# Kernel optimization log

Measured on AMD Instinct MI355X. Metric: run time of the kernel, lower is better.

The kernel has to match this reference:

```python
import jax, jax.numpy as jnp
import numpy as np

LM_TEMP = 2.0      # opts.lm_temp
LAMBDA_SH = 20.0   # lambda_sh passed in ot_loss
EPS = 1e-8


def sinkhorn(M, a, b, lam, num_iter_max=1000, stop_thr=0.005):
    """Faithful port of sinkhorn_pytorch. M:[S,V], a:[S,B], b:[V,B]."""
    K = jnp.exp(-M * lam)          # [S,V]
    KM = K * M
    u0 = jnp.ones_like(a) / a.shape[0]
    v0 = jnp.zeros_like(b)

    def cond(state):
        cpt, u, v, err = state
        return (cpt < num_iter_max) & (err > stop_thr)

    def body(state):
        cpt, u, v, err = state
        u = a / (K @ (b / (u.T @ K).T))   # fused fixed-point step
        cpt = cpt + 1
        do_check = ((cpt % 20) == 1) | (cpt == num_iter_max)

        def check(uve):
            u, v, _ = uve
            v = b / (K.T @ u)
            u = a / (K @ v)
            bb = v * (K.T @ u)
            err = jnp.max(jnp.sum(jnp.abs(bb - b), axis=0))  # inf-norm over batch
            return u, v, err

        u, v, err = jax.lax.cond(do_check, check, lambda t: t, (u, v, err))
        return cpt, u, v, err

    state0 = (jnp.asarray(0, jnp.int32), u0, v0, jnp.asarray(1.0, M.dtype))
    _, u, v, _ = jax.lax.while_loop(cond, body, state0)
    return jnp.sum(u * (KM @ v), axis=0)   # [B] sinkhorn divergences


def setup_inputs() -> dict:
    key = jax.random.key(0)
    ks = jax.random.split(key, 6)
    B, H, V, NV, MAX_SLOTS = 512, 1024, 28996, 3000, 33
    inputs = jax.random.normal(ks[0], (B, 2 * H), jnp.float32)
    outputs = jax.random.normal(ks[1], (B, 512), jnp.float32)
    W_lm = jax.random.normal(ks[2], (V, H), jnp.float32) * 0.02   # lm head (no bias)
    W_lin = jax.random.normal(ks[3], (MAX_SLOTS, 512), jnp.float32) * 0.05
    b_lin = jnp.zeros((MAX_SLOTS,), jnp.float32)
    topics = jax.random.normal(ks[4], (MAX_SLOTS - 1, H), jnp.float32) * 0.01
    verbs = jax.random.randint(ks[5], (NV,), 0, V)
    return {"inputs": inputs, "outputs": outputs, "W_lm": W_lm,
            "W_lin": W_lin, "b_lin": b_lin, "topics": topics,
            "verbs": verbs, "nslots": 33}


def reference(inputs, outputs, W_lm, W_lin, b_lin, topics, verbs, nslots):
    H = W_lm.shape[1]
    # gather verb rows of the lm head once: logits[:, verbs] == x @ W_lm[verbs].T
    W_v = W_lm[verbs]                               # [NV, H]
    Wt = W_v.T                                      # [H, NV]
    o11 = jax.nn.softmax((inputs[:, :H] @ Wt) / LM_TEMP, axis=-1)
    o12 = jax.nn.softmax((inputs[:, H:] @ Wt) / LM_TEMP, axis=-1)
    o1 = (o11 + o12) * 0.5
    o1 = o1 / jnp.sum(o1, axis=1, keepdims=True)    # [B, NV] vocab marginals
    o2 = jax.nn.softmax((outputs @ W_lin.T + b_lin)[:, 1:nslots], axis=-1)  # [B, S]
    # cosine-distance cost matrix between topics and verb embeddings
    tn = topics[:nslots - 1]
    tn = tn / (jnp.linalg.norm(tn, axis=1, keepdims=True) + EPS)
    vn = W_v / (jnp.linalg.norm(W_v, axis=1, keepdims=True) + EPS)
    M = 1.0 - tn @ vn.T                             # [S, NV]
    # single chunk of ot_loss (B <= 1024): mean sinkhorn divergence
    return jnp.mean(sinkhorn(M, o2.T, o1.T, LAMBDA_SH))
```

## Files before the change

kernel.cpp:

```cpp
#include <hip/hip_runtime.h>

#define NV 3000
#define HH 1024
#define BB 512

typedef __attribute__((ext_vector_type(8))) short short8;
typedef __attribute__((ext_vector_type(4))) float floatx4;

__device__ __forceinline__ float wave_sum(float x) {
#pragma unroll
  for (int off = 32; off; off >>= 1) x += __shfl_xor(x, off, 64);
  return x;
}
__device__ __forceinline__ unsigned bf16r(float x) {
  unsigned u = __float_as_uint(x);
  u += 0x7fffu + ((u >> 16) & 1u);
  return u >> 16;
}
__device__ __forceinline__ void gload16(const void* g, void* l) {
  __builtin_amdgcn_global_load_lds(
      (const __attribute__((address_space(1))) unsigned*)g,
      (__attribute__((address_space(3))) unsigned*)l, 16, 0, 0);
}

__device__ __forceinline__ void pk_fma_acc(float2& acc, float2 a, float2 b) {
  asm("v_pk_fma_f32 %0, %1, %2, %0" : "+v"(acc) : "v"(a), "v"(b));
}
__device__ __forceinline__ float2 unpk2(unsigned d) {
  float2 r;
  r.x = __uint_as_float(d << 16);
  r.y = __uint_as_float(d & 0xffff0000u);
  return r;
}

__global__ __launch_bounds__(256) void norms_wb_kernel(
    const float* __restrict__ W_lm, const float* __restrict__ topics,
    const int* __restrict__ verbs, float* __restrict__ vninv,
    float* __restrict__ tninv, unsigned short* __restrict__ Wb) {
  int r = blockIdx.x, t = threadIdx.x;
  bool isW = r < 3072;
  int j = isW ? (r < NV ? r : NV - 1) : 0;
  const float* src = isW ? (W_lm + (size_t)verbs[j] * HH)
                         : (topics + (size_t)(r - 3072) * HH);
  float4 v = *(const float4*)(src + t * 4);
  if (isW) {
    *(uint2*)(Wb + (size_t)r * HH + t * 4) =
        make_uint2(bf16r(v.x) | (bf16r(v.y) << 16),
                   bf16r(v.z) | (bf16r(v.w) << 16));
  }
  float ss = v.x * v.x + v.y * v.y + v.z * v.z + v.w * v.w;
  ss = wave_sum(ss);
  __shared__ float sq[4];
  if ((t & 63) == 0) sq[t >> 6] = ss;
  __syncthreads();
  if (t == 0) {
    float inv = 1.0f / (sqrtf(sq[0] + sq[1] + sq[2] + sq[3]) + 1e-8f);
    if (isW) { if (r < NV) vninv[r] = inv; }
    else tninv[r - 3072] = inv;
  }
}

__global__ __launch_bounds__(256) void xb_kernel(
    const float* __restrict__ inputs, unsigned short* __restrict__ Xb) {
  int idx = blockIdx.x * 256 + threadIdx.x;
  int r = idx >> 7, c8 = (idx & 127) << 3;
  const float* src = (r < 512) ? (inputs + (size_t)r * 2048 + c8)
                               : (inputs + (size_t)(r - 512) * 2048 + 1024 + c8);
  float4 x0 = ((const float4*)src)[0];
  float4 x1 = ((const float4*)src)[1];
  uint4 o;
  o.x = bf16r(x0.x) | (bf16r(x0.y) << 16);
  o.y = bf16r(x0.z) | (bf16r(x0.w) << 16);
  o.z = bf16r(x1.x) | (bf16r(x1.y) << 16);
  o.w = bf16r(x1.z) | (bf16r(x1.w) << 16);
  *(uint4*)(Xb + (size_t)r * HH + c8) = o;
}

__global__ __launch_bounds__(256) void topt_kernel(
    const float* __restrict__ topics, const float* __restrict__ tninv,
    float* __restrict__ topT) {
  int idx = blockIdx.x * 256 + threadIdx.x;
  int k = idx >> 5, s = idx & 31;
  topT[idx] = topics[(size_t)s * HH + k] * tninv[s];
}

__global__ __launch_bounds__(64) void a_kernel(
    const float* __restrict__ outputs, const float* __restrict__ W_lin,
    const float* __restrict__ b_lin, float* __restrict__ aT) {
  int r = blockIdx.x, t = threadIdx.x;
  __shared__ float orow[512];
  __shared__ float lg[33];
  __shared__ float ms[2];
  *(float4*)(orow + t * 8)     = *(const float4*)(outputs + (size_t)r * 512 + t * 8);
  *(float4*)(orow + t * 8 + 4) = *(const float4*)(outputs + (size_t)r * 512 + t * 8 + 4);
  __syncthreads();
  if (t < 33) {
    float acc = b_lin[t];
    for (int k = 0; k < 512; ++k) acc = fmaf(orow[k], W_lin[(size_t)t * 512 + k], acc);
    lg[t] = acc;
  }
  __syncthreads();
  if (t == 0) {
    float m = lg[1];
    for (int i = 2; i < 33; ++i) m = fmaxf(m, lg[i]);
    float ssum = 0.0f;
    for (int i = 1; i < 33; ++i) ssum += __expf(lg[i] - m);
    ms[0] = m; ms[1] = ssum;
  }
  __syncthreads();
  if (t >= 1 && t < 33) aT[(size_t)r * 32 + t - 1] = __expf(lg[t] - ms[0]) / ms[1];
}

__global__ __launch_bounds__(256) void gemm_mfma(
    const unsigned short* __restrict__ Xb, const unsigned short* __restrict__ Wb,
    float* __restrict__ L) {
  __shared__ unsigned short As[128 * 32], Bs[128 * 32];
  int t = threadIdx.x;
  int wave = t >> 6, ln = t & 63;
  int bn = blockIdx.x, bm = blockIdx.y;
  int wm = (wave >> 1) * 64, wn = (wave & 1) * 64;
  const unsigned short* ga = Xb + (size_t)(bm * 128 + (t >> 2)) * HH + (t & 3) * 8;
  const unsigned short* gb = Wb + (size_t)(bn * 128 + (t >> 2)) * HH + (t & 3) * 8;
  int lq = ln >> 4, lm = ln & 15;
  floatx4 acc[4][4];
#pragma unroll
  for (int i = 0; i < 4; ++i)
#pragma unroll
    for (int j = 0; j < 4; ++j) acc[i][j] = (floatx4)0.0f;

  for (int k0 = 0; k0 < HH; k0 += 32) {
    __syncthreads();
    gload16(ga + k0, As + t * 8);
    gload16(ga + (size_t)64 * HH + k0, As + 2048 + t * 8);
    gload16(gb + k0, Bs + t * 8);
    gload16(gb + (size_t)64 * HH + k0, Bs + 2048 + t * 8);
    __syncthreads();
    short8 af[4], bfr[4];
#pragma unroll
    for (int i = 0; i < 4; ++i)
      af[i] = *(const short8*)(As + (wm + i * 16 + lm) * 32 + lq * 8);
#pragma unroll
    for (int j = 0; j < 4; ++j)
      bfr[j] = *(const short8*)(Bs + (wn + j * 16 + lm) * 32 + lq * 8);
#pragma unroll
    for (int i = 0; i < 4; ++i)
#pragma unroll
      for (int j = 0; j < 4; ++j)
        acc[i][j] = __builtin_amdgcn_mfma_f32_16x16x32_bf16(af[i], bfr[j], acc[i][j], 0, 0, 0);
  }
  int row0 = bm * 128 + wm + lq * 4;
  int col0 = bn * 128 + wn + lm;
#pragma unroll
  for (int j = 0; j < 4; ++j) {
    int col = col0 + j * 16;
    if (col < NV) {
#pragma unroll
      for (int i = 0; i < 4; ++i) {
#pragma unroll
        for (int r = 0; r < 4; ++r)
          L[(size_t)(row0 + i * 16 + r) * NV + col] = acc[i][j][r] * 0.5f;
      }
    }
  }
}

__global__ __launch_bounds__(256) void softmax_kernel(
    float* __restrict__ L1, const float* __restrict__ L2) {
  int r = blockIdx.x, t = threadIdx.x, w = t >> 6, ln = t & 63;
  float* row1 = L1 + (size_t)r * NV;
  const float* row2 = L2 + (size_t)r * NV;
  __shared__ float rd[2][4];
  float s1 = 0.0f, s2 = 0.0f;
  for (int v = t; v < NV; v += 256) { s1 += __expf(row1[v]); s2 += __expf(row2[v]); }
  s1 = wave_sum(s1); s2 = wave_sum(s2);
  if (ln == 0) { rd[0][w] = s1; rd[1][w] = s2; }
  __syncthreads();
  s1 = rd[0][0] + rd[0][1] + rd[0][2] + rd[0][3];
  s2 = rd[1][0] + rd[1][1] + rd[1][2] + rd[1][3];
  float i1 = 0.5f / s1, i2 = 0.5f / s2;
  float rs = 0.0f;
  for (int v = t; v < NV; v += 256) {
    float o = __expf(row1[v]) * i1 + __expf(row2[v]) * i2;
    row1[v] = o; rs += o;
  }
  rs = wave_sum(rs);
  __syncthreads();
  if (ln == 0) rd[0][w] = rs;
  __syncthreads();
  float rinv = 1.0f / (rd[0][0] + rd[0][1] + rd[0][2] + rd[0][3]);
  for (int v = t; v < NV; v += 256) row1[v] *= rinv;
}

__global__ __launch_bounds__(256) void mk_kernel(
    const float* __restrict__ W_lm, const int* __restrict__ verbs,
    const float* __restrict__ topT, const float* __restrict__ vninv,
    unsigned* __restrict__ Kb, float* __restrict__ KMt) {
  __shared__ float red[4][64][33];
  int t = threadIdx.x, ln = t & 63, w = t >> 6;
  int v = blockIdx.x * 64 + ln;
  int vc = v < NV ? v : NV - 1;
  int kb = __builtin_amdgcn_readfirstlane(w) << 8;
  const float* wrow = W_lm + (size_t)verbs[vc] * HH + kb;
  const float* tb = topT + (size_t)kb * 32;
  float acc[32];
#pragma unroll
  for (int s = 0; s < 32; ++s) acc[s] = 0.0f;
  for (int kk = 0; kk < 256; kk += 4) {
    float4 w4 = *(const float4*)(wrow + kk);
    const float* tr = tb + kk * 32;
    const float* pw = (const float*)&w4;
#pragma unroll
    for (int d = 0; d < 4; ++d)
#pragma unroll
      for (int s = 0; s < 32; ++s) acc[s] = fmaf(pw[d], tr[d * 32 + s], acc[s]);
  }
#pragma unroll
  for (int s = 0; s < 32; ++s) red[w][ln][s] = acc[s];
  __syncthreads();
  for (int idx = t; idx < 1024; idx += 256) {
    int l = idx >> 4, pr = idx & 15;
    int vo = blockIdx.x * 64 + l;
    if (vo < NV) {
      int s0 = pr * 2, s1 = s0 + 1;
      float vi = vninv[vo];
      float d0 = red[0][l][s0] + red[1][l][s0] + red[2][l][s0] + red[3][l][s0];
      float d1 = red[0][l][s1] + red[1][l][s1] + red[2][l][s1] + red[3][l][s1];
      float M0 = 1.0f - d0 * vi, M1 = 1.0f - d1 * vi;
      float K0 = __expf(-20.0f * M0), K1 = __expf(-20.0f * M1);
      *(float2*)(KMt + (size_t)vo * 32 + s0) = make_float2(K0 * M0, K1 * M1);
      Kb[(size_t)vo * 16 + pr] = bf16r(K0) | (bf16r(K1) << 16);
    }
  }
}

__device__ __forceinline__ void gridbar(unsigned* bar, unsigned target) {
  __syncthreads();
  if (threadIdx.x == 0) {
    __hip_atomic_fetch_add(bar, 1u, __ATOMIC_RELEASE, __HIP_MEMORY_SCOPE_AGENT);
    while (__hip_atomic_load(bar, __ATOMIC_ACQUIRE, __HIP_MEMORY_SCOPE_AGENT) < target) {
      __builtin_amdgcn_s_sleep(1);
    }
  }
  __syncthreads();
}

template <bool STORE_T>
__device__ __forceinline__ void kpass_ss(
    const uint4* __restrict__ Kb, const float* __restrict__ bsh0,
    const float* __restrict__ bsh1, const float2* u0, const float2* u1,
    float2* z0, float2* z1, float* vsh0, float* vsh1, int pid, int p) {
#pragma unroll 3
  for (int i = 0; i < 6; ++i) {
    int v = pid + (i << 9);
    if (i < 5 || v < NV) {
      const uint4* kq = Kb + ((size_t)v << 2) + (p << 1);
      uint4 q0 = kq[0], q1 = kq[1];
      float2 kc[8];
      kc[0] = unpk2(q0.x); kc[1] = unpk2(q0.y);
      kc[2] = unpk2(q0.z); kc[3] = unpk2(q0.w);
      kc[4] = unpk2(q1.x); kc[5] = unpk2(q1.y);
      kc[6] = unpk2(q1.z); kc[7] = unpk2(q1.w);
      float2 w0 = make_float2(0.0f, 0.0f), w1 = make_float2(0.0f, 0.0f);
#pragma unroll
      for (int j = 0; j < 8; ++j) { pk_fma_acc(w0, kc[j], u0[j]); pk_fma_acc(w1, kc[j], u1[j]); }
      float s0 = w0.x + w0.y, s1 = w1.x + w1.y;
      s0 += __shfl_xor(s0, 1, 64);
      s1 += __shfl_xor(s1, 1, 64);
      float t0 = bsh0[v] * __builtin_amdgcn_rcpf(s0);
      float t1 = bsh1[v] * __builtin_amdgcn_rcpf(s1);
      if (STORE_T && !p) { vsh0[v] = t0; vsh1[v] = t1; }
      float2 t0p = make_float2(t0, t0), t1p = make_float2(t1, t1);
#pragma unroll
      for (int j = 0; j < 8; ++j) { pk_fma_acc(z0[j], kc[j], t0p); pk_fma_acc(z1[j], kc[j], t1p); }
    }
  }
}

__device__ __forceinline__ void errpass_ss(
    const uint4* __restrict__ Kb, const float* __restrict__ bsh0,
    const float* __restrict__ bsh1, const float2* u0, const float2* u1,
    const float* vsh0, const float* vsh1, float& ep0, float& ep1,
    int pid, int p) {
#pragma unroll 3
  for (int i = 0; i < 6; ++i) {
    int v = pid + (i << 9);
    if (i < 5 || v < NV) {
      const uint4* kq = Kb + ((size_t)v << 2) + (p << 1);
      uint4 q0 = kq[0], q1 = kq[1];
      float2 kc[8];
      kc[0] = unpk2(q0.x); kc[1] = unpk2(q0.y);
      kc[2] = unpk2(q0.z); kc[3] = unpk2(q0.w);
      kc[4] = unpk2(q1.x); kc[5] = unpk2(q1.y);
      kc[6] = unpk2(q1.z); kc[7] = unpk2(q1.w);
      float2 w0 = make_float2(0.0f, 0.0f), w1 = make_float2(0.0f, 0.0f);
#pragma unroll
      for (int j = 0; j < 8; ++j) { pk_fma_acc(w0, kc[j], u0[j]); pk_fma_acc(w1, kc[j], u1[j]); }
      float s0 = w0.x + w0.y, s1 = w1.x + w1.y;
      s0 += __shfl_xor(s0, 1, 64);
      s1 += __shfl_xor(s1, 1, 64);
      if (!p) {
        ep0 += fabsf(vsh0[v] * s0 - bsh0[v]);
        ep1 += fabsf(vsh1[v] * s1 - bsh1[v]);
      }
    }
  }
}

__device__ __forceinline__ float waveRS16(float* z, int ln) {
  int cnt = 16;
#pragma unroll
  for (int d = 2; d <= 16; d <<= 1) {
    int half = cnt >> 1;
    bool hi = (ln & d) != 0;
#pragma unroll
    for (int k = 0; k < 8; ++k) {
      if (k < half) {
        float a = z[k], b = z[half + k];
        z[k] = hi ? b : a;
        z[half + k] = hi ? a : b;
      }
    }
#pragma unroll
    for (int k = 0; k < 8; ++k)
      if (k < half) z[k] += __shfl_xor(z[half + k], d, 64);
    cnt = half;
  }
  return z[0] + __shfl_xor(z[0], 32, 64);
}

__global__ __launch_bounds__(1024) void sinkhorn_kernel(
    const uint4* __restrict__ Kb, const float* __restrict__ KMt,
    const float* __restrict__ bT, const float* __restrict__ aT,
    unsigned* __restrict__ slots, float* __restrict__ outp) {
  const int t = threadIdx.x;
  const int w = t >> 6, ln = t & 63;
  const int p = t & 1, pid = t >> 1;
  const int col0 = blockIdx.x << 1;
  const float* b0r = bT + (size_t)col0 * NV;
  const float* b1r = b0r + NV;
  float* accres = (float*)(slots + 64);
  unsigned* bar = slots + 65;

  __shared__ float zred[2][16][32];
  __shared__ float ush[2][32];
  __shared__ float sredA[16], sredB[16];
  __shared__ unsigned ebits;
  __shared__ float vsh0[3072], vsh1[3072];
  __shared__ float bsh0[3072], bsh1[3072];
  float* ushf = &ush[0][0];

  const int sl = ((ln & 1) << 4) | ((ln & 2) << 2) | (ln & 4) |
                 ((ln & 8) >> 2) | ((ln & 16) >> 4);

  for (int idx = t; idx < NV; idx += 1024) { bsh0[idx] = b0r[idx]; bsh1[idx] = b1r[idx]; }
  float areg = (t < 64) ? aT[(size_t)col0 * 32 + t] : 0.0f;

  float2 u0[8], u1[8];
#pragma unroll
  for (int j = 0; j < 8; ++j) {
    u0[j] = make_float2(1.0f / 32.0f, 1.0f / 32.0f);
    u1[j] = make_float2(1.0f / 32.0f, 1.0f / 32.0f);
  }
  if (t < 64) ushf[t] = 1.0f / 32.0f;
  __syncthreads();
  float err = 1.0f;
  int cpt = 0, chk = 0;
  unsigned barcnt = 0;

  while (cpt < 1000 && err > 0.005f) {
    float2 z0[8], z1[8];
#pragma unroll
    for (int j = 0; j < 8; ++j) { z0[j] = make_float2(0.0f, 0.0f); z1[j] = make_float2(0.0f, 0.0f); }
    kpass_ss<false>(Kb, bsh0, bsh1, u0, u1, z0, z1, vsh0, vsh1, pid, p);
    float r0 = waveRS16((float*)z0, ln), r1 = waveRS16((float*)z1, ln);
    __syncthreads();
    if (ln < 32) { zred[0][w][sl] = r0; zred[1][w][sl] = r1; }
    __syncthreads();
    if (t < 64) {
      int c = t >> 5, s = t & 31;
      float zz = 0.0f;
#pragma unroll
      for (int k = 0; k < 16; ++k) zz += zred[c][k][s];
      ushf[t] = areg * __builtin_amdgcn_rcpf(zz);
    }
    __syncthreads();
#pragma unroll
    for (int q = 0; q < 4; ++q) {
      *(float4*)((float*)u0 + q * 4) = *(float4*)(&ush[0][(p << 4) + q * 4]);
      *(float4*)((float*)u1 + q * 4) = *(float4*)(&ush[1][(p << 4) + q * 4]);
    }
    ++cpt;

    if (cpt % 20 == 1 || cpt == 1000) {
#pragma unroll
      for (int j = 0; j < 8; ++j) { z0[j] = make_float2(0.0f, 0.0f); z1[j] = make_float2(0.0f, 0.0f); }
      kpass_ss<true>(Kb, bsh0, bsh1, u0, u1, z0, z1, vsh0, vsh1, pid, p);
      r0 = waveRS16((float*)z0, ln); r1 = waveRS16((float*)z1, ln);
      __syncthreads();
      if (ln < 32) { zred[0][w][sl] = r0; zred[1][w][sl] = r1; }
      __syncthreads();
      if (t < 64) {
        int c = t >> 5, s = t & 31;
        float zz = 0.0f;
#pragma unroll
        for (int k = 0; k < 16; ++k) zz += zred[c][k][s];
        ushf[t] = areg * __builtin_amdgcn_rcpf(zz);
      }
      __syncthreads();
#pragma unroll
      for (int q = 0; q < 4; ++q) {
        *(float4*)((float*)u0 + q * 4) = *(float4*)(&ush[0][(p << 4) + q * 4]);
        *(float4*)((float*)u1 + q * 4) = *(float4*)(&ush[1][(p << 4) + q * 4]);
      }
      float ep0 = 0.0f, ep1 = 0.0f;
      errpass_ss(Kb, bsh0, bsh1, u0, u1, vsh0, vsh1, ep0, ep1, pid, p);
      ep0 = wave_sum(ep0); ep1 = wave_sum(ep1);
      if (ln == 0) { sredA[w] = ep0; sredB[w] = ep1; }
      __syncthreads();
      if (t == 0) {
        float e0 = 0.0f, e1 = 0.0f;
#pragma unroll
        for (int k = 0; k < 16; ++k) { e0 += sredA[k]; e1 += sredB[k]; }
        atomicMax(slots + chk, __float_as_uint(fmaxf(e0, e1)));
      }
      ++barcnt;
      gridbar(bar, barcnt * 256u);
      if (t == 0) ebits = __hip_atomic_load(slots + chk, __ATOMIC_RELAXED, __HIP_MEMORY_SCOPE_AGENT);
      __syncthreads();
      err = __uint_as_float(ebits);
      ++chk;
    }
  }

  float y0[16], y1[16];
#pragma unroll
  for (int s = 0; s < 16; ++s) { y0[s] = 0.0f; y1[s] = 0.0f; }
#pragma unroll 3
  for (int i = 0; i < 6; ++i) {
    int v = pid + (i << 9);
    if (i < 5 || v < NV) {
      const float4* kp = (const float4*)(KMt + (size_t)v * 32 + (p << 4));
      float kc[16];
#pragma unroll
      for (int q = 0; q < 4; ++q) *(float4*)(kc + q * 4) = kp[q];
      float x0 = vsh0[v], x1 = vsh1[v];
#pragma unroll
      for (int s = 0; s < 16; ++s) { y0[s] = fmaf(kc[s], x0, y0[s]); y1[s] = fmaf(kc[s], x1, y1[s]); }
    }
  }
  float r0 = waveRS16(y0, ln), r1 = waveRS16(y1, ln);
  __syncthreads();
  if (ln < 32) { zred[0][w][sl] = r0; zred[1][w][sl] = r1; }
  __syncthreads();
  if (t < 64) {
    int c = t >> 5, s = t & 31;
    float ys = 0.0f;
#pragma unroll
    for (int k = 0; k < 16; ++k) ys += zred[c][k][s];
    float pp = ys * ushf[t];
#pragma unroll
    for (int off = 1; off <= 16; off <<= 1) pp += __shfl_xor(pp, off, 64);
    float other = __shfl_xor(pp, 32, 64);
    if (t == 0) atomicAdd(accres, pp + other);
  }
  ++barcnt;
  gridbar(bar, barcnt * 256u);
  if (blockIdx.x == 0 && t == 0) {
    unsigned ab = __hip_atomic_load((unsigned*)accres, __ATOMIC_RELAXED, __HIP_MEMORY_SCOPE_AGENT);
    outp[0] = __uint_as_float(ab) / 512.0f;
  }
}

extern "C" void kernel_launch(void* const* d_in, const int* in_sizes, int n_in,
                              void* d_out, int out_size, void* d_ws, size_t ws_size,
                              hipStream_t stream) {
  (void)in_sizes; (void)n_in; (void)out_size; (void)ws_size;
  const float* inputs  = (const float*)d_in[0];
  const float* outputs = (const float*)d_in[1];
  const float* W_lm    = (const float*)d_in[2];
  const float* W_lin   = (const float*)d_in[3];
  const float* b_lin   = (const float*)d_in[4];
  const float* topics  = (const float*)d_in[5];
  const int*   verbs   = (const int*)d_in[6];
  float* out = (float*)d_out;

  char* ws = (char*)d_ws;
  float*    L     = (float*)(ws);
  float*    L1    = L;
  float*    L2    = (float*)(ws + 6144000);
  float*    aT    = (float*)(ws + 12288000);
  unsigned* Kb    = (unsigned*)(ws + 12353536);
  float*    KMt   = (float*)(ws + 12545536);
  float*    topT  = (float*)(ws + 12929536);
  float*    vninv = (float*)(ws + 13060608);
  float*    tninv = (float*)(ws + 13072640);
  unsigned* slots = (unsigned*)(ws + 13072768);
  unsigned short* Xb = (unsigned short*)(ws + 13073280);
  unsigned short* Wb = (unsigned short*)(ws + 15170432);

  hipMemsetAsync((void*)slots, 0, 512, stream);

  norms_wb_kernel<<<3104, 256, 0, stream>>>(W_lm, topics, verbs, vninv, tninv, Wb);
  xb_kernel<<<512, 256, 0, stream>>>(inputs, Xb);
  topt_kernel<<<128, 256, 0, stream>>>(topics, tninv, topT);
  a_kernel<<<BB, 64, 0, stream>>>(outputs, W_lin, b_lin, aT);
  gemm_mfma<<<dim3(24, 8), 256, 0, stream>>>(Xb, Wb, L);
  softmax_kernel<<<BB, 256, 0, stream>>>(L1, L2);
  mk_kernel<<<47, 256, 0, stream>>>(W_lm, verbs, topT, vninv, Kb, KMt);
  sinkhorn_kernel<<<256, 1024, 0, stream>>>((const uint4*)Kb, KMt, L1, aT, slots, out);
}
```

Baseline: 415.7 us.

## Stage most of bf16 K matrix in LDS and keep v values in registers

```diff
diff --git a/kernel.cpp b/kernel.cpp
--- a/kernel.cpp
+++ b/kernel.cpp
@@ -3,6 +3,7 @@
 #define NV 3000
 #define HH 1024
 #define BB 512
+#define KROWS_LDS 1920
 
 typedef __attribute__((ext_vector_type(8))) short short8;
 typedef __attribute__((ext_vector_type(4))) float floatx4;
@@ -244,64 +245,126 @@
   __syncthreads();
 }
 
+#define KROW_BODY(I, Q0, Q1, STORE)                                         \
+  {                                                                          \
+    float2 kc[8];                                                            \
+    kc[0] = unpk2((Q0).x); kc[1] = unpk2((Q0).y);                            \
+    kc[2] = unpk2((Q0).z); kc[3] = unpk2((Q0).w);                            \
+    kc[4] = unpk2((Q1).x); kc[5] = unpk2((Q1).y);                            \
+    kc[6] = unpk2((Q1).z); kc[7] = unpk2((Q1).w);                            \
+    float2 w0 = make_float2(0.f, 0.f), w1 = make_float2(0.f, 0.f);           \
+    _Pragma("unroll") for (int j = 0; j < 8; ++j) {                          \
+      pk_fma_acc(w0, kc[j], u0[j]); pk_fma_acc(w1, kc[j], u1[j]);            \
+    }                                                                        \
+    float s0 = w0.x + w0.y, s1 = w1.x + w1.y;                                \
+    s0 += __shfl_xor(s0, 1, 64);                                             \
+    s1 += __shfl_xor(s1, 1, 64);                                             \
+    float t0 = bsh0[v] * __builtin_amdgcn_rcpf(s0);                          \
+    float t1 = bsh1[v] * __builtin_amdgcn_rcpf(s1);                          \
+    if (STORE) { tr0[I] = t0; tr1[I] = t1; }                                 \
+    float2 t0p = make_float2(t0, t0), t1p = make_float2(t1, t1);             \
+    _Pragma("unroll") for (int j = 0; j < 8; ++j) {                          \
+      pk_fma_acc(z0[j], kc[j], t0p); pk_fma_acc(z1[j], kc[j], t1p);          \
+    }                                                                        \
+  }
+
 template <bool STORE_T>
 __device__ __forceinline__ void kpass_ss(
-    const uint4* __restrict__ Kb, const float* __restrict__ bsh0,
-    const float* __restrict__ bsh1, const float2* u0, const float2* u1,
-    float2* z0, float2* z1, float* vsh0, float* vsh1, int pid, int p) {
-#pragma unroll 3
-  for (int i = 0; i < 6; ++i) {
+    const uint4* __restrict__ Kb, const unsigned short* Ksh,
+    const float* __restrict__ bsh0, const float* __restrict__ bsh1,
+    const float2* u0, const float2* u1, float2* z0, float2* z1,
+    float* tr0, float* tr1, int pid, int p) {
+#pragma unroll
+  for (int i = 0; i < 3; ++i) {
     int v = pid + (i << 9);
-    if (i < 5 || v < NV) {
+    const uint4* kq = (const uint4*)(Ksh + ((size_t)v << 5) + (p << 4));
+    uint4 q0 = kq[0], q1 = kq[1];
+    KROW_BODY(i, q0, q1, STORE_T)
+  }
+  {
+    int v = pid + 1536;
+    uint4 q0, q1;
+    if (v < KROWS_LDS) {
+      const uint4* kq = (const uint4*)(Ksh + ((size_t)v << 5) + (p << 4));
+      q0 = kq[0]; q1 = kq[1];
+    } else {
+      const uint4* kq = Kb + ((size_t)v << 2) + (p << 1);
+      q0 = kq[0]; q1 = kq[1];
+    }
+    KROW_BODY(3, q0, q1, STORE_T)
+  }
+  {
+    int v = pid + 2048;
+    const uint4* kq = Kb + ((size_t)v << 2) + (p << 1);
+    uint4 q0 = kq[0], q1 = kq[1];
+    KROW_BODY(4, q0, q1, STORE_T)
+  }
+  {
+    int v = pid + 2560;
+    if (v < NV) {
       const uint4* kq = Kb + ((size_t)v << 2) + (p << 1);
       uint4 q0 = kq[0], q1 = kq[1];
-      float2 kc[8];
-      kc[0] = unpk2(q0.x); kc[1] = unpk2(q0.y);
-      kc[2] = unpk2(q0.z); kc[3] = unpk2(q0.w);
-      kc[4] = unpk2(q1.x); kc[5] = unpk2(q1.y);
-      kc[6] = unpk2(q1.z); kc[7] = unpk2(q1.w);
-      float2 w0 = make_float2(0.0f, 0.0f), w1 = make_float2(0.0f, 0.0f);
-#pragma unroll
-      for (int j = 0; j < 8; ++j) { pk_fma_acc(w0, kc[j], u0[j]); pk_fma_acc(w1, kc[j], u1[j]); }
-      float s0 = w0.x + w0.y, s1 = w1.x + w1.y;
-      s0 += __shfl_xor(s0, 1, 64);
-      s1 += __shfl_xor(s1, 1, 64);
-      float t0 = bsh0[v] * __builtin_amdgcn_rcpf(s0);
-      float t1 = bsh1[v] * __builtin_amdgcn_rcpf(s1);
-      if (STORE_T && !p) { vsh0[v] = t0; vsh1[v] = t1; }
-      float2 t0p = make_float2(t0, t0), t1p = make_float2(t1, t1);
-#pragma unroll
-      for (int j = 0; j < 8; ++j) { pk_fma_acc(z0[j], kc[j], t0p); pk_fma_acc(z1[j], kc[j], t1p); }
-    }
-  }
-}
+      KROW_BODY(5, q0, q1, STORE_T)
+    }
+  }
+}
+
+#define EROW_BODY(I, Q0, Q1)                                                 \
+  {                                                                          \
+    float2 kc[8];                                                            \
+    kc[0] = unpk2((Q0).x); kc[1] = unpk2((Q0).y);                            \
+    kc[2] = unpk2((Q0).z); kc[3] = unpk2((Q0).w);                            \
+    kc[4] = unpk2((Q1).x); kc[5] = unpk2((Q1).y);                            \
+    kc[6] = unpk2((Q1).z); kc[7] = unpk2((Q1).w);                            \
+    float2 w0 = make_float2(0.f, 0.f), w1 = make_float2(0.f, 0.f);           \
+    _Pragma("unroll") for (int j = 0; j < 8; ++j) {                          \
+      pk_fma_acc(w0, kc[j], u0[j]); pk_fma_acc(w1, kc[j], u1[j]);            \
+    }                                                                        \
+    float s0 = w0.x + w0.y, s1 = w1.x + w1.y;                                \
+    s0 += __shfl_xor(s0, 1, 64);                                             \
+    s1 += __shfl_xor(s1, 1, 64);                                             \
+    if (!p) {                                                                \
+      ep0 += fabsf(tr0[I] * s0 - bsh0[v]);                                   \
+      ep1 += fabsf(tr1[I] * s1 - bsh1[v]);                                   \
+    }                                                                        \
+  }
 
 __device__ __forceinline__ void errpass_ss(
-    const uint4* __restrict__ Kb, const float* __restrict__ bsh0,
-    const float* __restrict__ bsh1, const float2* u0, const float2* u1,
-    const float* vsh0, const float* vsh1, float& ep0, float& ep1,
-    int pid, int p) {
-#pragma unroll 3
-  for (int i = 0; i < 6; ++i) {
+    const uint4* __restrict__ Kb, const unsigned short* Ksh,
+    const float* __restrict__ bsh0, const float* __restrict__ bsh1,
+    const float2* u0, const float2* u1, const float* tr0, const float* tr1,
+    float& ep0, float& ep1, int pid, int p) {
+#pragma unroll
+  for (int i = 0; i < 3; ++i) {
     int v = pid + (i << 9);
-    if (i < 5 || v < NV) {
+    const uint4* kq = (const uint4*)(Ksh + ((size_t)v << 5) + (p << 4));
+    uint4 q0 = kq[0], q1 = kq[1];
+    EROW_BODY(i, q0, q1)
+  }
+  {
+    int v = pid + 1536;
+    uint4 q0, q1;
+    if (v < KROWS_LDS) {
+      const uint4* kq = (const uint4*)(Ksh + ((size_t)v << 5) + (p << 4));
+      q0 = kq[0]; q1 = kq[1];
+    } else {
+      const uint4* kq = Kb + ((size_t)v << 2) + (p << 1);
+      q0 = kq[0]; q1 = kq[1];
+    }
+    EROW_BODY(3, q0, q1)
+  }
+  {
+    int v = pid + 2048;
+    const uint4* kq = Kb + ((size_t)v << 2) + (p << 1);
+    uint4 q0 = kq[0], q1 = kq[1];
+    EROW_BODY(4, q0, q1)
+  }
+  {
+    int v = pid + 2560;
+    if (v < NV) {
       const uint4* kq = Kb + ((size_t)v << 2) + (p << 1);
       uint4 q0 = kq[0], q1 = kq[1];
-      float2 kc[8];
-      kc[0] = unpk2(q0.x); kc[1] = unpk2(q0.y);
-      kc[2] = unpk2(q0.z); kc[3] = unpk2(q0.w);
-      kc[4] = unpk2(q1.x); kc[5] = unpk2(q1.y);
-      kc[6] = unpk2(q1.z); kc[7] = unpk2(q1.w);
-      float2 w0 = make_float2(0.0f, 0.0f), w1 = make_float2(0.0f, 0.0f);
-#pragma unroll
-      for (int j = 0; j < 8; ++j) { pk_fma_acc(w0, kc[j], u0[j]); pk_fma_acc(w1, kc[j], u1[j]); }
-      float s0 = w0.x + w0.y, s1 = w1.x + w1.y;
-      s0 += __shfl_xor(s0, 1, 64);
-      s1 += __shfl_xor(s1, 1, 64);
-      if (!p) {
-        ep0 += fabsf(vsh0[v] * s0 - bsh0[v]);
-        ep1 += fabsf(vsh1[v] * s1 - bsh1[v]);
-      }
+      EROW_BODY(5, q0, q1)
     }
   }
 }
@@ -341,14 +404,21 @@
   float* accres = (float*)(slots + 64);
   unsigned* bar = slots + 65;
 
+  __shared__ __align__(16) unsigned short Ksh[KROWS_LDS * 32];
   __shared__ float zred[2][16][32];
   __shared__ float ush[2][32];
   __shared__ float sredA[16], sredB[16];
   __shared__ unsigned ebits;
-  __shared__ float vsh0[3072], vsh1[3072];
   __shared__ float bsh0[3072], bsh1[3072];
   float* ushf = &ush[0][0];
 
+#pragma unroll
+  for (int s = 0; s < 8; ++s) {
+    int off = (s << 14) + t * 16;
+    if (off < KROWS_LDS * 64)
+      gload16((const char*)Kb + off, (char*)Ksh + off);
+  }
+
   const int sl = ((ln & 1) << 4) | ((ln & 2) << 2) | (ln & 4) |
                  ((ln & 8) >> 2) | ((ln & 16) >> 4);
 
@@ -356,11 +426,14 @@
   float areg = (t < 64) ? aT[(size_t)col0 * 32 + t] : 0.0f;
 
   float2 u0[8], u1[8];
+  float tr0[6], tr1[6];
 #pragma unroll
   for (int j = 0; j < 8; ++j) {
     u0[j] = make_float2(1.0f / 32.0f, 1.0f / 32.0f);
     u1[j] = make_float2(1.0f / 32.0f, 1.0f / 32.0f);
   }
+#pragma unroll
+  for (int j = 0; j < 6; ++j) { tr0[j] = 0.0f; tr1[j] = 0.0f; }
   if (t < 64) ushf[t] = 1.0f / 32.0f;
   __syncthreads();
   float err = 1.0f;
@@ -371,9 +444,8 @@
     float2 z0[8], z1[8];
 #pragma unroll
     for (int j = 0; j < 8; ++j) { z0[j] = make_float2(0.0f, 0.0f); z1[j] = make_float2(0.0f, 0.0f); }
-    kpass_ss<false>(Kb, bsh0, bsh1, u0, u1, z0, z1, vsh0, vsh1, pid, p);
+    kpass_ss<false>(Kb, Ksh, bsh0, bsh1, u0, u1, z0, z1, tr0, tr1, pid, p);
     float r0 = waveRS16((float*)z0, ln), r1 = waveRS16((float*)z1, ln);
-    __syncthreads();
     if (ln < 32) { zred[0][w][sl] = r0; zred[1][w][sl] = r1; }
     __syncthreads();
     if (t < 64) {
@@ -394,9 +466,8 @@
     if (cpt % 20 == 1 || cpt == 1000) {
 #pragma unroll
       for (int j = 0; j < 8; ++j) { z0[j] = make_float2(0.0f, 0.0f); z1[j] = make_float2(0.0f, 0.0f); }
-      kpass_ss<true>(Kb, bsh0, bsh1, u0, u1, z0, z1, vsh0, vsh1, pid, p);
+      kpass_ss<true>(Kb, Ksh, bsh0, bsh1, u0, u1, z0, z1, tr0, tr1, pid, p);
       r0 = waveRS16((float*)z0, ln); r1 = waveRS16((float*)z1, ln);
-      __syncthreads();
       if (ln < 32) { zred[0][w][sl] = r0; zred[1][w][sl] = r1; }
       __syncthreads();
       if (t < 64) {
@@ -413,7 +484,7 @@
         *(float4*)((float*)u1 + q * 4) = *(float4*)(&ush[1][(p << 4) + q * 4]);
       }
       float ep0 = 0.0f, ep1 = 0.0f;
-      errpass_ss(Kb, bsh0, bsh1, u0, u1, vsh0, vsh1, ep0, ep1, pid, p);
+      errpass_ss(Kb, Ksh, bsh0, bsh1, u0, u1, tr0, tr1, ep0, ep1, pid, p);
       ep0 = wave_sum(ep0); ep1 = wave_sum(ep1);
       if (ln == 0) { sredA[w] = ep0; sredB[w] = ep1; }
       __syncthreads();
@@ -435,7 +506,7 @@
   float y0[16], y1[16];
 #pragma unroll
   for (int s = 0; s < 16; ++s) { y0[s] = 0.0f; y1[s] = 0.0f; }
-#pragma unroll 3
+#pragma unroll
   for (int i = 0; i < 6; ++i) {
     int v = pid + (i << 9);
     if (i < 5 || v < NV) {
@@ -443,7 +514,7 @@
       float kc[16];
 #pragma unroll
       for (int q = 0; q < 4; ++q) *(float4*)(kc + q * 4) = kp[q];
-      float x0 = vsh0[v], x1 = vsh1[v];
+      float x0 = tr0[i], x1 = tr1[i];
 #pragma unroll
       for (int s = 0; s < 16; ++s) { y0[s] = fmaf(kc[s], x0, y0[s]); y1[s] = fmaf(kc[s], x1, y1[s]); }
     }
```

New measurement: 432.5 us. 4.0% more time.

## Cache half of K in registers and cut per-iteration block barriers to one

Applied to the files above, without the earlier changes.

```diff
diff --git a/kernel.cpp b/kernel.cpp
--- a/kernel.cpp
+++ b/kernel.cpp
@@ -246,21 +246,27 @@
 
 template <bool STORE_T>
 __device__ __forceinline__ void kpass_ss(
-    const uint4* __restrict__ Kb, const float* __restrict__ bsh0,
-    const float* __restrict__ bsh1, const float2* u0, const float2* u1,
-    float2* z0, float2* z1, float* vsh0, float* vsh1, int pid, int p) {
-#pragma unroll 3
+    const uint4* __restrict__ Kb, const uint4* kr,
+    const float* __restrict__ bsh0, const float* __restrict__ bsh1,
+    const float2* u0, const float2* u1, float2* z0, float2* z1,
+    float* vsh0, float* vsh1, int pid, int p) {
+#pragma unroll
   for (int i = 0; i < 6; ++i) {
     int v = pid + (i << 9);
     if (i < 5 || v < NV) {
-      const uint4* kq = Kb + ((size_t)v << 2) + (p << 1);
-      uint4 q0 = kq[0], q1 = kq[1];
+      uint4 q0, q1;
+      if (i < 3) {
+        q0 = kr[2 * i]; q1 = kr[2 * i + 1];
+      } else {
+        const uint4* kq = Kb + ((size_t)v << 2) + (p << 1);
+        q0 = kq[0]; q1 = kq[1];
+      }
       float2 kc[8];
       kc[0] = unpk2(q0.x); kc[1] = unpk2(q0.y);
       kc[2] = unpk2(q0.z); kc[3] = unpk2(q0.w);
       kc[4] = unpk2(q1.x); kc[5] = unpk2(q1.y);
       kc[6] = unpk2(q1.z); kc[7] = unpk2(q1.w);
-      float2 w0 = make_float2(0.0f, 0.0f), w1 = make_float2(0.0f, 0.0f);
+      float2 w0 = make_float2(0.f, 0.f), w1 = make_float2(0.f, 0.f);
 #pragma unroll
       for (int j = 0; j < 8; ++j) { pk_fma_acc(w0, kc[j], u0[j]); pk_fma_acc(w1, kc[j], u1[j]); }
       float s0 = w0.x + w0.y, s1 = w1.x + w1.y;
@@ -277,22 +283,28 @@
 }
 
 __device__ __forceinline__ void errpass_ss(
-    const uint4* __restrict__ Kb, const float* __restrict__ bsh0,
-    const float* __restrict__ bsh1, const float2* u0, const float2* u1,
+    const uint4* __restrict__ Kb, const uint4* kr,
+    const float* __restrict__ bsh0, const float* __restrict__ bsh1,
+    const float2* u0, const float2* u1,
     const float* vsh0, const float* vsh1, float& ep0, float& ep1,
     int pid, int p) {
-#pragma unroll 3
+#pragma unroll
   for (int i = 0; i < 6; ++i) {
     int v = pid + (i << 9);
     if (i < 5 || v < NV) {
-      const uint4* kq = Kb + ((size_t)v << 2) + (p << 1);
-      uint4 q0 = kq[0], q1 = kq[1];
+      uint4 q0, q1;
+      if (i < 3) {
+        q0 = kr[2 * i]; q1 = kr[2 * i + 1];
+      } else {
+        const uint4* kq = Kb + ((size_t)v << 2) + (p << 1);
+        q0 = kq[0]; q1 = kq[1];
+      }
       float2 kc[8];
       kc[0] = unpk2(q0.x); kc[1] = unpk2(q0.y);
       kc[2] = unpk2(q0.z); kc[3] = unpk2(q0.w);
       kc[4] = unpk2(q1.x); kc[5] = unpk2(q1.y);
       kc[6] = unpk2(q1.z); kc[7] = unpk2(q1.w);
-      float2 w0 = make_float2(0.0f, 0.0f), w1 = make_float2(0.0f, 0.0f);
+      float2 w0 = make_float2(0.f, 0.f), w1 = make_float2(0.f, 0.f);
 #pragma unroll
       for (int j = 0; j < 8; ++j) { pk_fma_acc(w0, kc[j], u0[j]); pk_fma_acc(w1, kc[j], u1[j]); }
       float s0 = w0.x + w0.y, s1 = w1.x + w1.y;
@@ -341,19 +353,25 @@
   float* accres = (float*)(slots + 64);
   unsigned* bar = slots + 65;
 
-  __shared__ float zred[2][16][32];
-  __shared__ float ush[2][32];
+  __shared__ float zred[2][2][16][32];
+  __shared__ __align__(16) float ushw[16 * 64];
   __shared__ float sredA[16], sredB[16];
   __shared__ unsigned ebits;
   __shared__ float vsh0[3072], vsh1[3072];
   __shared__ float bsh0[3072], bsh1[3072];
-  float* ushf = &ush[0][0];
 
   const int sl = ((ln & 1) << 4) | ((ln & 2) << 2) | (ln & 4) |
                  ((ln & 8) >> 2) | ((ln & 16) >> 4);
 
   for (int idx = t; idx < NV; idx += 1024) { bsh0[idx] = b0r[idx]; bsh1[idx] = b1r[idx]; }
-  float areg = (t < 64) ? aT[(size_t)col0 * 32 + t] : 0.0f;
+  const float areg = aT[(size_t)col0 * 32 + ln];
+
+  uint4 kr[6];
+#pragma unroll
+  for (int i = 0; i < 3; ++i) {
+    const uint4* kq = Kb + ((size_t)(pid + (i << 9)) << 2) + (p << 1);
+    kr[2 * i] = kq[0]; kr[2 * i + 1] = kq[1];
+  }
 
   float2 u0[8], u1[8];
 #pragma unroll
@@ -361,59 +379,47 @@
     u0[j] = make_float2(1.0f / 32.0f, 1.0f / 32.0f);
     u1[j] = make_float2(1.0f / 32.0f, 1.0f / 32.0f);
   }
-  if (t < 64) ushf[t] = 1.0f / 32.0f;
   __syncthreads();
   float err = 1.0f;
-  int cpt = 0, chk = 0;
+  int cpt = 0, chk = 0, zb = 0;
   unsigned barcnt = 0;
+
+  auto ured = [&]() {
+    int c = ln >> 5, s = ln & 31;
+    float zz = 0.0f;
+#pragma unroll
+    for (int k = 0; k < 16; ++k) zz += zred[zb][c][k][s];
+    float uu = areg * __builtin_amdgcn_rcpf(zz);
+    ushw[(w << 6) + ln] = uu;
+#pragma unroll
+    for (int q = 0; q < 4; ++q) {
+      *(float4*)((float*)u0 + q * 4) = *(float4*)(&ushw[(w << 6) + (p << 4) + q * 4]);
+      *(float4*)((float*)u1 + q * 4) = *(float4*)(&ushw[(w << 6) + 32 + (p << 4) + q * 4]);
+    }
+    zb ^= 1;
+  };
 
   while (cpt < 1000 && err > 0.005f) {
     float2 z0[8], z1[8];
 #pragma unroll
     for (int j = 0; j < 8; ++j) { z0[j] = make_float2(0.0f, 0.0f); z1[j] = make_float2(0.0f, 0.0f); }
-    kpass_ss<false>(Kb, bsh0, bsh1, u0, u1, z0, z1, vsh0, vsh1, pid, p);
+    kpass_ss<false>(Kb, kr, bsh0, bsh1, u0, u1, z0, z1, vsh0, vsh1, pid, p);
     float r0 = waveRS16((float*)z0, ln), r1 = waveRS16((float*)z1, ln);
+    if (ln < 32) { zred[zb][0][w][sl] = r0; zred[zb][1][w][sl] = r1; }
     __syncthreads();
-    if (ln < 32) { zred[0][w][sl] = r0; zred[1][w][sl] = r1; }
-    __syncthreads();
-    if (t < 64) {
-      int c = t >> 5, s = t & 31;
-      float zz = 0.0f;
-#pragma unroll
-      for (int k = 0; k < 16; ++k) zz += zred[c][k][s];
-      ushf[t] = areg * __builtin_amdgcn_rcpf(zz);
-    }
-    __syncthreads();
-#pragma unroll
-    for (int q = 0; q < 4; ++q) {
-      *(float4*)((float*)u0 + q * 4) = *(float4*)(&ush[0][(p << 4) + q * 4]);
-      *(float4*)((float*)u1 + q * 4) = *(float4*)(&ush[1][(p << 4) + q * 4]);
-    }
+    ured();
     ++cpt;
 
     if (cpt % 20 == 1 || cpt == 1000) {
 #pragma unroll
       for (int j = 0; j < 8; ++j) { z0[j] = make_float2(0.0f, 0.0f); z1[j] = make_float2(0.0f, 0.0f); }
-      kpass_ss<true>(Kb, bsh0, bsh1, u0, u1, z0, z1, vsh0, vsh1, pid, p);
+      kpass_ss<true>(Kb, kr, bsh0, bsh1, u0, u1, z0, z1, vsh0, vsh1, pid, p);
       r0 = waveRS16((float*)z0, ln); r1 = waveRS16((float*)z1, ln);
+      if (ln < 32) { zred[zb][0][w][sl] = r0; zred[zb][1][w][sl] = r1; }
       __syncthreads();
-      if (ln < 32) { zred[0][w][sl] = r0; zred[1][w][sl] = r1; }
-      __syncthreads();
-      if (t < 64) {
-        int c = t >> 5, s = t & 31;
-        float zz = 0.0f;
-#pragma unroll
-        for (int k = 0; k < 16; ++k) zz += zred[c][k][s];
-        ushf[t] = areg * __builtin_amdgcn_rcpf(zz);
-      }
-      __syncthreads();
-#pragma unroll
-      for (int q = 0; q < 4; ++q) {
-        *(float4*)((float*)u0 + q * 4) = *(float4*)(&ush[0][(p << 4) + q * 4]);
-        *(float4*)((float*)u1 + q * 4) = *(float4*)(&ush[1][(p << 4) + q * 4]);
-      }
+      ured();
       float ep0 = 0.0f, ep1 = 0.0f;
-      errpass_ss(Kb, bsh0, bsh1, u0, u1, vsh0, vsh1, ep0, ep1, pid, p);
+      errpass_ss(Kb, kr, bsh0, bsh1, u0, u1, vsh0, vsh1, ep0, ep1, pid, p);
       ep0 = wave_sum(ep0); ep1 = wave_sum(ep1);
       if (ln == 0) { sredA[w] = ep0; sredB[w] = ep1; }
       __syncthreads();
@@ -435,7 +441,7 @@
   float y0[16], y1[16];
 #pragma unroll
   for (int s = 0; s < 16; ++s) { y0[s] = 0.0f; y1[s] = 0.0f; }
-#pragma unroll 3
+#pragma unroll
   for (int i = 0; i < 6; ++i) {
     int v = pid + (i << 9);
     if (i < 5 || v < NV) {
@@ -450,14 +456,14 @@
   }
   float r0 = waveRS16(y0, ln), r1 = waveRS16(y1, ln);
   __syncthreads();
-  if (ln < 32) { zred[0][w][sl] = r0; zred[1][w][sl] = r1; }
+  if (ln < 32) { zred[0][0][w][sl] = r0; zred[0][1][w][sl] = r1; }
   __syncthreads();
   if (t < 64) {
     int c = t >> 5, s = t & 31;
     float ys = 0.0f;
 #pragma unroll
-    for (int k = 0; k < 16; ++k) ys += zred[c][k][s];
-    float pp = ys * ushf[t];
+    for (int k = 0; k < 16; ++k) ys += zred[0][c][k][s];
+    float pp = ys * ushw[t];
 #pragma unroll
     for (int off = 1; off <= 16; off <<= 1) pp += __shfl_xor(pp, off, 64);
     float other = __shfl_xor(pp, 32, 64);
```

New measurement: 570.2 us. +37.2%, slower.

## Cut barriers per Sinkhorn iteration via redundant per-wave u reduction and double-buffered zred

Applied to the files above, without the earlier changes.

```diff
diff --git a/kernel.cpp b/kernel.cpp
--- a/kernel.cpp
+++ b/kernel.cpp
@@ -260,7 +260,7 @@
       kc[2] = unpk2(q0.z); kc[3] = unpk2(q0.w);
       kc[4] = unpk2(q1.x); kc[5] = unpk2(q1.y);
       kc[6] = unpk2(q1.z); kc[7] = unpk2(q1.w);
-      float2 w0 = make_float2(0.0f, 0.0f), w1 = make_float2(0.0f, 0.0f);
+      float2 w0 = make_float2(0.f, 0.f), w1 = make_float2(0.f, 0.f);
 #pragma unroll
       for (int j = 0; j < 8; ++j) { pk_fma_acc(w0, kc[j], u0[j]); pk_fma_acc(w1, kc[j], u1[j]); }
       float s0 = w0.x + w0.y, s1 = w1.x + w1.y;
@@ -292,7 +292,7 @@
       kc[2] = unpk2(q0.z); kc[3] = unpk2(q0.w);
       kc[4] = unpk2(q1.x); kc[5] = unpk2(q1.y);
       kc[6] = unpk2(q1.z); kc[7] = unpk2(q1.w);
-      float2 w0 = make_float2(0.0f, 0.0f), w1 = make_float2(0.0f, 0.0f);
+      float2 w0 = make_float2(0.f, 0.f), w1 = make_float2(0.f, 0.f);
 #pragma unroll
       for (int j = 0; j < 8; ++j) { pk_fma_acc(w0, kc[j], u0[j]); pk_fma_acc(w1, kc[j], u1[j]); }
       float s0 = w0.x + w0.y, s1 = w1.x + w1.y;
@@ -327,6 +327,21 @@
   }
   return z[0] + __shfl_xor(z[0], 32, 64);
 }
+
+#define URED()                                                               \
+  {                                                                          \
+    int c_ = ln >> 5, s_ = ln & 31;                                          \
+    float zz_ = 0.0f;                                                        \
+    _Pragma("unroll") for (int k_ = 0; k_ < 16; ++k_)                        \
+        zz_ += zred[zb][c_][k_][s_];                                         \
+    float uu_ = areg * __builtin_amdgcn_rcpf(zz_);                           \
+    ushw[(w << 6) + ln] = uu_;                                               \
+    _Pragma("unroll") for (int j_ = 0; j_ < 8; ++j_) {                       \
+      u0[j_] = *(const float2*)(&ushw[(w << 6) + (p << 4) + 2 * j_]);        \
+      u1[j_] = *(const float2*)(&ushw[(w << 6) + 32 + (p << 4) + 2 * j_]);   \
+    }                                                                        \
+    zb ^= 1;                                                                 \
+  }
 
 __global__ __launch_bounds__(1024) void sinkhorn_kernel(
     const uint4* __restrict__ Kb, const float* __restrict__ KMt,
@@ -341,19 +356,18 @@
   float* accres = (float*)(slots + 64);
   unsigned* bar = slots + 65;
 
-  __shared__ float zred[2][16][32];
-  __shared__ float ush[2][32];
+  __shared__ float zred[2][2][16][32];
+  __shared__ __align__(16) float ushw[16 * 64];
   __shared__ float sredA[16], sredB[16];
   __shared__ unsigned ebits;
   __shared__ float vsh0[3072], vsh1[3072];
   __shared__ float bsh0[3072], bsh1[3072];
-  float* ushf = &ush[0][0];
 
   const int sl = ((ln & 1) << 4) | ((ln & 2) << 2) | (ln & 4) |
                  ((ln & 8) >> 2) | ((ln & 16) >> 4);
 
   for (int idx = t; idx < NV; idx += 1024) { bsh0[idx] = b0r[idx]; bsh1[idx] = b1r[idx]; }
-  float areg = (t < 64) ? aT[(size_t)col0 * 32 + t] : 0.0f;
+  const float areg = aT[(size_t)col0 * 32 + ln];
 
   float2 u0[8], u1[8];
 #pragma unroll
@@ -361,10 +375,9 @@
     u0[j] = make_float2(1.0f / 32.0f, 1.0f / 32.0f);
     u1[j] = make_float2(1.0f / 32.0f, 1.0f / 32.0f);
   }
-  if (t < 64) ushf[t] = 1.0f / 32.0f;
   __syncthreads();
   float err = 1.0f;
-  int cpt = 0, chk = 0;
+  int cpt = 0, chk = 0, zb = 0;
   unsigned barcnt = 0;
 
   while (cpt < 1000 && err > 0.005f) {
@@ -373,22 +386,9 @@
     for (int j = 0; j < 8; ++j) { z0[j] = make_float2(0.0f, 0.0f); z1[j] = make_float2(0.0f, 0.0f); }
     kpass_ss<false>(Kb, bsh0, bsh1, u0, u1, z0, z1, vsh0, vsh1, pid, p);
     float r0 = waveRS16((float*)z0, ln), r1 = waveRS16((float*)z1, ln);
+    if (ln < 32) { zred[zb][0][w][sl] = r0; zred[zb][1][w][sl] = r1; }
     __syncthreads();
-    if (ln < 32) { zred[0][w][sl] = r0; zred[1][w][sl] = r1; }
-    __syncthreads();
-    if (t < 64) {
-      int c = t >> 5, s = t & 31;
-      float zz = 0.0f;
-#pragma unroll
-      for (int k = 0; k < 16; ++k) zz += zred[c][k][s];
-      ushf[t] = areg * __builtin_amdgcn_rcpf(zz);
-    }
-    __syncthreads();
-#pragma unroll
-    for (int q = 0; q < 4; ++q) {
-      *(float4*)((float*)u0 + q * 4) = *(float4*)(&ush[0][(p << 4) + q * 4]);
-      *(float4*)((float*)u1 + q * 4) = *(float4*)(&ush[1][(p << 4) + q * 4]);
-    }
+    URED();
     ++cpt;
 
     if (cpt % 20 == 1 || cpt == 1000) {
@@ -396,22 +396,9 @@
       for (int j = 0; j < 8; ++j) { z0[j] = make_float2(0.0f, 0.0f); z1[j] = make_float2(0.0f, 0.0f); }
       kpass_ss<true>(Kb, bsh0, bsh1, u0, u1, z0, z1, vsh0, vsh1, pid, p);
       r0 = waveRS16((float*)z0, ln); r1 = waveRS16((float*)z1, ln);
+      if (ln < 32) { zred[zb][0][w][sl] = r0; zred[zb][1][w][sl] = r1; }
       __syncthreads();
-      if (ln < 32) { zred[0][w][sl] = r0; zred[1][w][sl] = r1; }
-      __syncthreads();
-      if (t < 64) {
-        int c = t >> 5, s = t & 31;
-        float zz = 0.0f;
-#pragma unroll
-        for (int k = 0; k < 16; ++k) zz += zred[c][k][s];
-        ushf[t] = areg * __builtin_amdgcn_rcpf(zz);
-      }
-      __syncthreads();
-#pragma unroll
-      for (int q = 0; q < 4; ++q) {
-        *(float4*)((float*)u0 + q * 4) = *(float4*)(&ush[0][(p << 4) + q * 4]);
-        *(float4*)((float*)u1 + q * 4) = *(float4*)(&ush[1][(p << 4) + q * 4]);
-      }
+      URED();
       float ep0 = 0.0f, ep1 = 0.0f;
       errpass_ss(Kb, bsh0, bsh1, u0, u1, vsh0, vsh1, ep0, ep1, pid, p);
       ep0 = wave_sum(ep0); ep1 = wave_sum(ep1);
@@ -450,14 +437,14 @@
   }
   float r0 = waveRS16(y0, ln), r1 = waveRS16(y1, ln);
   __syncthreads();
-  if (ln < 32) { zred[0][w][sl] = r0; zred[1][w][sl] = r1; }
+  if (ln < 32) { zred[0][0][w][sl] = r0; zred[0][1][w][sl] = r1; }
   __syncthreads();
   if (t < 64) {
     int c = t >> 5, s = t & 31;
     float ys = 0.0f;
 #pragma unroll
-    for (int k = 0; k < 16; ++k) ys += zred[c][k][s];
-    float pp = ys * ushf[t];
+    for (int k = 0; k < 16; ++k) ys += zred[0][c][k][s];
+    float pp = ys * ushw[t];
 #pragma unroll
     for (int off = 1; off <= 16; off <<= 1) pp += __shfl_xor(pp, off, 64);
     float other = __shfl_xor(pp, 32, 64);
```

After: 426.7 us. +2.6%, slower.
